# Optimization experiments

Hardware: AMD Instinct MI355X
Metric: run time of the kernel (lower is better)

The kernel has to match this reference:

```python
import jax, jax.numpy as jnp
import numpy as np

POOL = 7
IMAGE_SHAPE = (1024, 1024)
NUM_CLASSES = 81
BN_EPS = 1e-5


def _crop_and_resize(feat, boxes, P):
    """tf.image.crop_and_resize-style bilinear crop. feat: (B,C,H,W), boxes: (B,N,4) normalized [y1,x1,y2,x2]. Returns (B,N,C,P,P)."""
    B, C, H, W = feat.shape

    def one(f, bx):
        ff = f.reshape(C, H * W)
        y1, x1, y2, x2 = bx[:, 0], bx[:, 1], bx[:, 2], bx[:, 3]
        t = jnp.linspace(0.0, 1.0, P)
        ys = (y1[:, None] + (y2 - y1)[:, None] * t) * (H - 1)  # (N,P)
        xs = (x1[:, None] + (x2 - x1)[:, None] * t) * (W - 1)
        y0 = jnp.floor(ys)
        x0 = jnp.floor(xs)
        wy = (ys - y0)[None, :, :, None]  # broadcast to (1,N,P,1)
        wx = (xs - x0)[None, :, None, :]  # (1,N,1,P)
        yi0 = jnp.clip(y0, 0, H - 1).astype(jnp.int32)
        yi1 = jnp.clip(y0 + 1, 0, H - 1).astype(jnp.int32)
        xi0 = jnp.clip(x0, 0, W - 1).astype(jnp.int32)
        xi1 = jnp.clip(x0 + 1, 0, W - 1).astype(jnp.int32)

        def g(yi, xi):
            return ff[:, yi[:, :, None] * W + xi[:, None, :]]  # (C,N,P,P)

        out = (g(yi0, xi0) * (1 - wy) * (1 - wx) + g(yi0, xi1) * (1 - wy) * wx
               + g(yi1, xi0) * wy * (1 - wx) + g(yi1, xi1) * wy * wx)
        return jnp.transpose(out, (1, 0, 2, 3))  # (N,C,P,P)

    return jax.vmap(one)(feat, boxes)


def _pyramid_roi_align(rois, feats, P, image_shape):
    h = rois[..., 2] - rois[..., 0]
    w = rois[..., 3] - rois[..., 1]
    scale = 224.0 / np.sqrt(float(image_shape[0] * image_shape[1]))
    lvl = jnp.log2(jnp.sqrt(jnp.maximum(h * w, 1e-12)) / scale)
    level = jnp.clip(4 + jnp.round(lvl).astype(jnp.int32), 2, 5)  # (B,N)
    pooled = 0.0
    for i, f in enumerate(feats):  # levels 2..5
        mask = (level == (i + 2))[..., None, None, None].astype(f.dtype)
        pooled = pooled + mask * _crop_and_resize(f, rois, P)
    return pooled  # (B,N,C,P,P)


def _bn_relu(x, gamma, beta):
    # training-mode BatchNorm per batch slice (batch_slice => stats over the n_rois dim)
    mu = jnp.mean(x, axis=1, keepdims=True)
    var = jnp.mean((x - mu) ** 2, axis=1, keepdims=True)
    return jax.nn.relu(gamma * (x - mu) / jnp.sqrt(var + BN_EPS) + beta)


def setup_inputs() -> dict:
    key = jax.random.key(0)
    ks = jax.random.split(key, 16)
    B, N, C, F, K = 2, 1000, 256, 1024, NUM_CLASSES
    p = jax.random.uniform(ks[0], (B, N, 4), dtype=jnp.float32)
    yy = jnp.sort(p[..., 0:2], axis=-1)
    xx = jnp.sort(p[..., 2:4], axis=-1)
    rois = jnp.stack([yy[..., 0], xx[..., 0], yy[..., 1], xx[..., 1]], axis=-1)
    inp = {
        'rois': rois,
        'p2': jax.random.normal(ks[1], (B, C, 256, 256), dtype=jnp.float32),
        'p3': jax.random.normal(ks[2], (B, C, 128, 128), dtype=jnp.float32),
        'p4': jax.random.normal(ks[3], (B, C, 64, 64), dtype=jnp.float32),
        'p5': jax.random.normal(ks[4], (B, C, 32, 32), dtype=jnp.float32),
        'conv1_w': jax.random.normal(ks[5], (F, C, POOL, POOL), dtype=jnp.float32) * 0.02,
        'conv1_b': jnp.zeros((F,), jnp.float32),
        'bn1_g': jnp.ones((F,), jnp.float32),
        'bn1_b': jnp.zeros((F,), jnp.float32),
        'conv2_w': jax.random.normal(ks[6], (F, F), dtype=jnp.float32) * 0.02,
        'conv2_b': jnp.zeros((F,), jnp.float32),
        'bn2_g': jnp.ones((F,), jnp.float32),
        'bn2_b': jnp.zeros((F,), jnp.float32),
        'logits_w': jax.random.normal(ks[7], (K, F), dtype=jnp.float32) * 0.02,
        'logits_b': jnp.zeros((K,), jnp.float32),
        'bbox_w': jax.random.normal(ks[8], (K * 4, F), dtype=jnp.float32) * 0.02,
        'bbox_b': jnp.zeros((K * 4,), jnp.float32),
    }
    return inp


def reference(rois, p2, p3, p4, p5, conv1_w, conv1_b, bn1_g, bn1_b,
              conv2_w, conv2_b, bn2_g, bn2_b, logits_w, logits_b, bbox_w, bbox_b):
    B, N = rois.shape[0], rois.shape[1]
    pooled = _pyramid_roi_align(rois, [p2, p3, p4, p5], POOL, IMAGE_SHAPE)  # (B,N,C,P,P)
    # conv1: kernel == pool size => full contraction to 1x1 spatial
    x = jnp.einsum('bnchw,fchw->bnf', pooled, conv1_w) + conv1_b
    x = _bn_relu(x, bn1_g, bn1_b)
    # conv2: 1x1 conv == matmul
    x = x @ conv2_w.T + conv2_b
    shared = _bn_relu(x, bn2_g, bn2_b)  # (B,N,F)
    logits = shared @ logits_w.T + logits_b  # (B,N,K)
    probs = jax.nn.softmax(logits, axis=-1)
    bbox = (shared @ bbox_w.T + bbox_b).reshape(B, N, NUM_CLASSES, 4)
    return (logits, probs, bbox)
```

## Files before the change

kernel.cpp:

```cpp
#include <hip/hip_runtime.h>
#include <cstdint>
#include <cstddef>

typedef _Float16 H16;
typedef _Float16 half8 __attribute__((ext_vector_type(8)));
typedef float f32x4 __attribute__((ext_vector_type(4)));

typedef __attribute__((address_space(1))) const unsigned int gu32;
typedef __attribute__((address_space(3))) unsigned int lu32;
__device__ __forceinline__ void glds16(const void* g, void* l) {
  __builtin_amdgcn_global_load_lds((gu32*)g, (lu32*)l, 16, 0, 0);
}

__global__ __launch_bounds__(256) void k_transpose(const float* __restrict__ in,
                                                   H16* __restrict__ out,
                                                   int H, int W) {
  __shared__ float t[32 * 257];
  const int tid = threadIdx.x;
  const int w0 = blockIdx.x * 32;
  const int h  = blockIdx.y;
  const int b  = blockIdx.z;
  const size_t HW = (size_t)H * W;
  const int cL = tid >> 3;
  const int w4 = (tid & 7) * 4;
  const float* src = in + (size_t)b * 256 * HW + (size_t)h * W + w0;
#pragma unroll
  for (int i = 0; i < 8; ++i) {
    const int c = i * 32 + cL;
    const float4 v = *(const float4*)(src + (size_t)c * HW + w4);
    t[(w4 + 0) * 257 + c] = v.x;
    t[(w4 + 1) * 257 + c] = v.y;
    t[(w4 + 2) * 257 + c] = v.z;
    t[(w4 + 3) * 257 + c] = v.w;
  }
  __syncthreads();
  const int wS = (tid & 3) * 8;
  const int c4 = (tid >> 2) * 4;
  H16* dst = out + ((size_t)b * H + h) * W * 256;
#pragma unroll
  for (int j = 0; j < 8; ++j) {
    const int w = wS + j;
    const float a0 = t[w * 257 + c4 + 0];
    const float a1 = t[w * 257 + c4 + 1];
    const float a2 = t[w * 257 + c4 + 2];
    const float a3 = t[w * 257 + c4 + 3];
    union { H16 hh[4]; uint2 u; } r;
    r.hh[0] = (H16)a0; r.hh[1] = (H16)a1; r.hh[2] = (H16)a2; r.hh[3] = (H16)a3;
    *(uint2*)(dst + (size_t)(w0 + w) * 256 + c4) = r.u;
  }
}

__global__ __launch_bounds__(256) void k_prep_w1(const float* __restrict__ w,
                                                 H16* __restrict__ wt) {
  const int f = blockIdx.x;
  __shared__ __align__(16) H16 l[12544];
  const float* wf = w + (size_t)f * 12544;
  for (int e = threadIdx.x; e < 12544; e += 256) {
    const int cc = e / 49, pp = e % 49;
    l[pp * 256 + cc] = (H16)wf[e];
  }
  __syncthreads();
  H16* of = wt + (size_t)f * 12544;
  for (int ch = threadIdx.x; ch < 1568; ch += 256) {
    *(uint4*)(of + ch * 8) = *(const uint4*)(l + ch * 8);
  }
}

__global__ __launch_bounds__(256) void k_cast_f16(const float4* __restrict__ in,
                                                  uint2* __restrict__ out, int n4) {
  const int i = blockIdx.x * 256 + threadIdx.x;
  if (i >= n4) return;
  const float4 v = in[i];
  union { H16 hh[4]; uint2 u; } r;
  r.hh[0] = (H16)v.x; r.hh[1] = (H16)v.y; r.hh[2] = (H16)v.z; r.hh[3] = (H16)v.w;
  out[i] = r.u;
}

__global__ __launch_bounds__(256) void k_prep_w3(const float4* __restrict__ lw,
                                                 const float4* __restrict__ bw,
                                                 uint2* __restrict__ out) {
  const int i = blockIdx.x * 256 + threadIdx.x;
  const int r = (i * 4) >> 10;
  float4 v;
  if (r < 81)       v = lw[i];
  else if (r < 405) v = bw[i - 20736];
  else              v = make_float4(0.f, 0.f, 0.f, 0.f);
  union { H16 hh[4]; uint2 u; } rr;
  rr.hh[0] = (H16)v.x; rr.hh[1] = (H16)v.y; rr.hh[2] = (H16)v.z; rr.hh[3] = (H16)v.w;
  out[i] = rr.u;
}

__global__ __launch_bounds__(256) void k_roialign(const float* __restrict__ rois,
    const H16* __restrict__ f2, const H16* __restrict__ f3,
    const H16* __restrict__ f4p, const H16* __restrict__ f5,
    H16* __restrict__ pooled) {
  const int m = blockIdx.x;
  const int g  = threadIdx.x >> 6;
  const int c4 = (threadIdx.x & 63) * 4;
  H16* outp = pooled + (size_t)m * 12544 + c4;
  if (m >= 2000) {
    const uint2 z = make_uint2(0u, 0u);
    for (int p = g; p < 49; p += 4) *(uint2*)(outp + p * 256) = z;
    return;
  }
  const int b = (m >= 1000) ? 1 : 0;
  const float y1v = rois[m * 4 + 0], x1v = rois[m * 4 + 1];
  const float y2v = rois[m * 4 + 2], x2v = rois[m * 4 + 3];
  const float dy = y2v - y1v, dx = x2v - x1v;
  const float area = fmaxf(dy * dx, 1e-12f);
  const float lvl = log2f(sqrtf(area) / 0.21875f);
  int level = 4 + (int)rintf(lvl);
  level = level < 2 ? 2 : (level > 5 ? 5 : level);
  const H16* ft; int H;
  if (level == 2)      { ft = f2; H = 256; }
  else if (level == 3) { ft = f3; H = 128; }
  else if (level == 4) { ft = f4p; H = 64; }
  else                 { ft = f5; H = 32; }
  const float Hm1 = (float)(H - 1);
  const size_t bbase = (size_t)b * H * H * 256;
#pragma unroll 1
  for (int p = g; p < 49; p += 4) {
    const int py = (p * 147) >> 10;
    const int px = p - py * 7;
    const float ys = (y1v + dy * (py * 0.16666667f)) * Hm1;
    const float xs = (x1v + dx * (px * 0.16666667f)) * Hm1;
    const float yf = floorf(ys), xf = floorf(xs);
    const float wyv = ys - yf, wxv = xs - xf;
    int yi = (int)yf, xi = (int)xf;
    yi = yi < 0 ? 0 : (yi > H - 1 ? H - 1 : yi);
    xi = xi < 0 ? 0 : (xi > H - 1 ? H - 1 : xi);
    const int yiB = (yi + 1 > H - 1) ? H - 1 : yi + 1;
    const int xiB = (xi + 1 > H - 1) ? H - 1 : xi + 1;
    const size_t r0 = bbase + (size_t)yi * H * 256;
    const size_t r1 = bbase + (size_t)yiB * H * 256;
    union { uint2 u; H16 hh[4]; } v00, v01, v10, v11;
    v00.u = *(const uint2*)(ft + r0 + (size_t)xi  * 256 + c4);
    v01.u = *(const uint2*)(ft + r0 + (size_t)xiB * 256 + c4);
    v10.u = *(const uint2*)(ft + r1 + (size_t)xi  * 256 + c4);
    v11.u = *(const uint2*)(ft + r1 + (size_t)xiB * 256 + c4);
    const float w00 = (1.f - wyv) * (1.f - wxv);
    const float w01 = (1.f - wyv) * wxv;
    const float w10 = wyv * (1.f - wxv);
    const float w11 = wyv * wxv;
    union { H16 hh[4]; uint2 u; } r;
#pragma unroll
    for (int q = 0; q < 4; ++q) {
      const float val = (float)v00.hh[q] * w00 + (float)v01.hh[q] * w01
                      + (float)v10.hh[q] * w10 + (float)v11.hh[q] * w11;
      r.hh[q] = (H16)val;
    }
    *(uint2*)(outp + p * 256) = r.u;
  }
}

__global__ __launch_bounds__(256) void k_gemm(const H16* __restrict__ A,
                                              const H16* __restrict__ Bw,
                                              float* __restrict__ Cout,
                                              int Nn, int Ktot, int kchunk) {
  __shared__ __align__(16) H16 As[128 * 32];
  __shared__ __align__(16) H16 Bs[128 * 32];
  const int m0 = blockIdx.x * 128;
  const int n0 = blockIdx.y * 128;
  const int k0 = blockIdx.z * kchunk;
  float* __restrict__ Cp = Cout + (size_t)blockIdx.z * ((size_t)2048 * Nn);
  const int tid  = threadIdx.x;
  const int lane = tid & 63;
  const int wave = tid >> 6;
  const int wm = (wave >> 1) * 64;
  const int wn = (wave & 1) * 64;
  const int r1 = tid >> 2;
  const int cb = (tid & 3) * 8;
  const H16* gA1 = A  + (size_t)(m0 + r1) * Ktot + cb + k0;
  const H16* gA2 = A  + (size_t)(m0 + 64 + r1) * Ktot + cb + k0;
  const H16* gB1 = Bw + (size_t)(n0 + r1) * Ktot + cb + k0;
  const H16* gB2 = Bw + (size_t)(n0 + 64 + r1) * Ktot + cb + k0;
  H16* lA1 = As + tid * 8;
  H16* lA2 = As + 2048 + tid * 8;
  H16* lB1 = Bs + tid * 8;
  H16* lB2 = Bs + 2048 + tid * 8;
  f32x4 acc[4][4];
#pragma unroll
  for (int i = 0; i < 4; ++i)
#pragma unroll
    for (int j = 0; j < 4; ++j) acc[i][j] = (f32x4){0.f, 0.f, 0.f, 0.f};
  const int fr = lane & 15, fk = (lane >> 4) * 8;
  const int niter = kchunk >> 5;
  for (int it = 0; it < niter; ++it) {
    __syncthreads();
    glds16(gA1, lA1); glds16(gA2, lA2);
    glds16(gB1, lB1); glds16(gB2, lB2);
    gA1 += 32; gA2 += 32; gB1 += 32; gB2 += 32;
    __syncthreads();
    half8 af[4], bf[4];
#pragma unroll
    for (int i = 0; i < 4; ++i) af[i] = *(const half8*)(As + (wm + i * 16 + fr) * 32 + fk);
#pragma unroll
    for (int i = 0; i < 4; ++i) bf[i] = *(const half8*)(Bs + (wn + i * 16 + fr) * 32 + fk);
#pragma unroll
    for (int i = 0; i < 4; ++i)
#pragma unroll
      for (int j = 0; j < 4; ++j)
        acc[i][j] = __builtin_amdgcn_mfma_f32_16x16x32_f16(af[i], bf[j], acc[i][j], 0, 0, 0);
  }
  const int fq = lane >> 4;
#pragma unroll
  for (int i = 0; i < 4; ++i)
#pragma unroll
    for (int j = 0; j < 4; ++j) {
      const int col = n0 + wn + j * 16 + fr;
#pragma unroll
      for (int q = 0; q < 4; ++q) {
        const int row = m0 + wm + i * 16 + fq * 4 + q;
        Cp[(size_t)row * Nn + col] = acc[i][j][q];
      }
    }
}

__global__ __launch_bounds__(256) void k_reduce4(const float4* __restrict__ part,
                                                 float4* __restrict__ x1) {
  const int i = blockIdx.x * 256 + threadIdx.x;
  const float4 a = part[i], b = part[i + 524288], c = part[i + 1048576], d = part[i + 1572864];
  float4 r;
  r.x = a.x + b.x + c.x + d.x; r.y = a.y + b.y + c.y + d.y;
  r.z = a.z + b.z + c.z + d.z; r.w = a.w + b.w + c.w + d.w;
  x1[i] = r;
}

__global__ __launch_bounds__(256) void k_bn_stats(const float* __restrict__ X,
                                                  float* __restrict__ psum,
                                                  float* __restrict__ psq) {
  const int nc = blockIdx.x;
  const int b  = blockIdx.y;
  const int f4 = threadIdx.x * 4;
  const float* xp = X + (size_t)(b * 1000 + nc * 40) * 1024 + f4;
  float4 s = {0.f, 0.f, 0.f, 0.f}, q = {0.f, 0.f, 0.f, 0.f};
  for (int r = 0; r < 40; ++r) {
    const float4 v = *(const float4*)(xp + (size_t)r * 1024);
    s.x += v.x; s.y += v.y; s.z += v.z; s.w += v.w;
    q.x += v.x * v.x; q.y += v.y * v.y; q.z += v.z * v.z; q.w += v.w * v.w;
  }
  const size_t o = (size_t)(b * 25 + nc) * 1024 + f4;
  *(float4*)(psum + o) = s;
  *(float4*)(psq + o)  = q;
}

__global__ __launch_bounds__(256) void k_bn_fin(const float* __restrict__ psum,
                                                const float* __restrict__ psq,
                                                const float* __restrict__ gamma,
                                                const float* __restrict__ beta,
                                                float* __restrict__ coeff) {
  const int idx = blockIdx.x * 256 + threadIdx.x;
  const int b = idx >> 10, f = idx & 1023;
  float S = 0.f, Q = 0.f;
  for (int i = 0; i < 25; ++i) {
    S += psum[(size_t)(b * 25 + i) * 1024 + f];
    Q += psq[(size_t)(b * 25 + i) * 1024 + f];
  }
  const float mu   = S * 0.001f;
  const float var  = Q * 0.001f - mu * mu;
  const float rstd = rsqrtf(var + 1e-5f);
  const float a = gamma[f] * rstd;
  coeff[idx * 2]     = a;
  coeff[idx * 2 + 1] = beta[f] - mu * a;
}

__global__ __launch_bounds__(256) void k_bn_apply(const float* __restrict__ X,
                                                  const float* __restrict__ coeff,
                                                  H16* __restrict__ Y) {
  const int idx = blockIdx.x * 256 + threadIdx.x;
  const int m  = idx >> 8;
  const int f4 = (idx & 255) * 4;
  union { H16 hh[4]; uint2 u; } r;
  if (m >= 2000) {
    r.hh[0] = r.hh[1] = r.hh[2] = r.hh[3] = (H16)0.f;
    *(uint2*)(Y + (size_t)idx * 4) = r.u;
    return;
  }
  const int b = (m >= 1000) ? 1 : 0;
  const float4 v   = *(const float4*)(X + (size_t)idx * 4);
  const float4 c01 = *(const float4*)(coeff + b * 2048 + f4 * 2);
  const float4 c23 = *(const float4*)(coeff + b * 2048 + f4 * 2 + 4);
  r.hh[0] = (H16)fmaxf(c01.x * v.x + c01.y, 0.f);
  r.hh[1] = (H16)fmaxf(c01.z * v.y + c01.w, 0.f);
  r.hh[2] = (H16)fmaxf(c23.x * v.z + c23.y, 0.f);
  r.hh[3] = (H16)fmaxf(c23.z * v.w + c23.w, 0.f);
  *(uint2*)(Y + (size_t)idx * 4) = r.u;
}

__global__ __launch_bounds__(64) void k_head(const float* __restrict__ Z,
                                             const float* __restrict__ lb,
                                             const float* __restrict__ bb,
                                             float* __restrict__ out) {
  const int m = blockIdx.x;
  const int lane = threadIdx.x;
  const float* zr = Z + (size_t)m * 512;
  float* outL = out;
  float* outP = out + 162000;
  float* outB = out + 324000;
  const float v0 = zr[lane] + lb[lane];
  const float v1 = (lane < 17) ? (zr[64 + lane] + lb[64 + lane]) : -3.0e38f;
  outL[(size_t)m * 81 + lane] = v0;
  if (lane < 17) outL[(size_t)m * 81 + 64 + lane] = v1;
  float mx = fmaxf(v0, v1);
#pragma unroll
  for (int off = 32; off > 0; off >>= 1) mx = fmaxf(mx, __shfl_xor(mx, off));
  const float e0 = expf(v0 - mx);
  const float e1 = (lane < 17) ? expf(v1 - mx) : 0.f;
  float sm = e0 + e1;
#pragma unroll
  for (int off = 32; off > 0; off >>= 1) sm += __shfl_xor(sm, off);
  const float inv = 1.0f / sm;
  outP[(size_t)m * 81 + lane] = e0 * inv;
  if (lane < 17) outP[(size_t)m * 81 + 64 + lane] = e1 * inv;
#pragma unroll
  for (int j = 0; j < 6; ++j) {
    const int cc = lane + j * 64;
    if (cc < 324) outB[(size_t)m * 324 + cc] = zr[81 + cc] + bb[cc];
  }
}

extern "C" void kernel_launch(void* const* d_in, const int* in_sizes, int n_in,
                              void* d_out, int out_size, void* d_ws, size_t ws_size,
                              hipStream_t stream) {
  char* ws = (char*)d_ws;
  H16* fT2    = (H16*)(ws);
  H16* fT3    = (H16*)(ws + 67108864);
  H16* fT4    = (H16*)(ws + 83886080);
  H16* fT5    = (H16*)(ws + 88080384);
  H16* w1t    = (H16*)(ws + 89128960);
  H16* pooled = (H16*)(ws + 114819072);
  float* part  = (float*)(ws);
  float* x1    = (float*)(ws + 33554432);
  float* zz    = (float*)(ws + 41943040);
  H16*   y1    = (H16*)(ws + 67108864);
  float* x2    = (float*)(ws + 71303168);
  H16*   y2    = (H16*)(ws + 79691776);
  H16*   w2b   = (H16*)(ws + 83886080);
  H16*   w3b   = (H16*)(ws + 85983232);
  float* psum  = (float*)(ws + 87031808);
  float* psq   = (float*)(ws + 87236608);
  float* coef1 = (float*)(ws + 87441408);
  float* coef2 = (float*)(ws + 87457792);

  const float* rois = (const float*)d_in[0];

  k_transpose<<<dim3(8, 256, 2), 256, 0, stream>>>((const float*)d_in[1], fT2, 256, 256);
  k_transpose<<<dim3(4, 128, 2), 256, 0, stream>>>((const float*)d_in[2], fT3, 128, 128);
  k_transpose<<<dim3(2,  64, 2), 256, 0, stream>>>((const float*)d_in[3], fT4,  64,  64);
  k_transpose<<<dim3(1,  32, 2), 256, 0, stream>>>((const float*)d_in[4], fT5,  32,  32);
  k_prep_w1<<<1024, 256, 0, stream>>>((const float*)d_in[5], w1t);
  k_roialign<<<2048, 256, 0, stream>>>(rois, fT2, fT3, fT4, fT5, pooled);
  k_cast_f16<<<1024, 256, 0, stream>>>((const float4*)d_in[9], (uint2*)w2b, 262144);
  k_prep_w3<<<512, 256, 0, stream>>>((const float4*)d_in[13], (const float4*)d_in[15], (uint2*)w3b);

  k_gemm<<<dim3(16, 8, 4), 256, 0, stream>>>(pooled, w1t, part, 1024, 12544, 3136);
  k_reduce4<<<2048, 256, 0, stream>>>((const float4*)part, (float4*)x1);

  k_bn_stats<<<dim3(25, 2), 256, 0, stream>>>(x1, psum, psq);
  k_bn_fin<<<8, 256, 0, stream>>>(psum, psq, (const float*)d_in[7], (const float*)d_in[8], coef1);
  k_bn_apply<<<2048, 256, 0, stream>>>(x1, coef1, y1);

  k_gemm<<<dim3(16, 8, 1), 256, 0, stream>>>(y1, w2b, x2, 1024, 1024, 1024);

  k_bn_stats<<<dim3(25, 2), 256, 0, stream>>>(x2, psum, psq);
  k_bn_fin<<<8, 256, 0, stream>>>(psum, psq, (const float*)d_in[11], (const float*)d_in[12], coef2);
  k_bn_apply<<<2048, 256, 0, stream>>>(x2, coef2, y2);

  k_gemm<<<dim3(16, 4, 1), 256, 0, stream>>>(y2, w3b, zz, 512, 1024, 1024);
  k_head<<<2000, 64, 0, stream>>>(zz, (const float*)d_in[14], (const float*)d_in[16], (float*)d_out);
}
```

Before: 527.8 us.

## Increase split-K for all GEMMs, fuse reduction with BN stats, merge launches

The four per-level transposes become one launch, with a write pattern that stores each row contiguously, and the two small weight casts become one launch. The conv1 GEMM moves from 4 to 8 K-splits, and conv2 and the head GEMM get 4 K-splits each. The split-K partials are then summed inside a combined reduce+BN-stats kernel or inside the head kernel. The LDS padding in the w1 prep is changed to avoid bank conflicts. This is meant to fill more CUs during the small GEMMs and to cut launch count and extra passes over memory, at the cost of more partial-sum traffic.

```diff
diff --git a/kernel.cpp b/kernel.cpp
--- a/kernel.cpp
+++ b/kernel.cpp
@@ -12,18 +12,29 @@
   __builtin_amdgcn_global_load_lds((gu32*)g, (lu32*)l, 16, 0, 0);
 }
 
-__global__ __launch_bounds__(256) void k_transpose(const float* __restrict__ in,
-                                                   H16* __restrict__ out,
-                                                   int H, int W) {
+__global__ __launch_bounds__(256) void k_transpose_all(
+    const float* __restrict__ p2, const float* __restrict__ p3,
+    const float* __restrict__ p4, const float* __restrict__ p5,
+    H16* __restrict__ o2, H16* __restrict__ o3,
+    H16* __restrict__ o4, H16* __restrict__ o5) {
   __shared__ float t[32 * 257];
   const int tid = threadIdx.x;
-  const int w0 = blockIdx.x * 32;
-  const int h  = blockIdx.y;
-  const int b  = blockIdx.z;
-  const size_t HW = (size_t)H * W;
+  int bid = blockIdx.x;
+  const float* in; H16* out; int H;
+  if (bid < 4096)      { in = p2; out = o2; H = 256; }
+  else if (bid < 5120) { in = p3; out = o3; H = 128; bid -= 4096; }
+  else if (bid < 5376) { in = p4; out = o4; H = 64;  bid -= 5120; }
+  else                 { in = p5; out = o5; H = 32;  bid -= 5376; }
+  const int wpb = H >> 5;
+  const int strips = wpb * H;
+  const int b = (bid >= strips) ? 1 : 0;
+  bid -= b ? strips : 0;
+  const int h = bid / wpb;
+  const int w0 = (bid - h * wpb) * 32;
+  const size_t HW = (size_t)H * H;
   const int cL = tid >> 3;
   const int w4 = (tid & 7) * 4;
-  const float* src = in + (size_t)b * 256 * HW + (size_t)h * W + w0;
+  const float* src = in + (size_t)b * 256 * HW + (size_t)h * H + w0;
 #pragma unroll
   for (int i = 0; i < 8; ++i) {
     const int c = i * 32 + cL;
@@ -34,60 +45,60 @@
     t[(w4 + 3) * 257 + c] = v.w;
   }
   __syncthreads();
-  const int wS = (tid & 3) * 8;
-  const int c4 = (tid >> 2) * 4;
-  H16* dst = out + ((size_t)b * H + h) * W * 256;
+  const int wS = tid >> 6;
+  const int c4 = (tid & 63) * 4;
+  H16* dst = out + (((size_t)b * H + h) * H + w0) * 256;
 #pragma unroll
   for (int j = 0; j < 8; ++j) {
-    const int w = wS + j;
-    const float a0 = t[w * 257 + c4 + 0];
-    const float a1 = t[w * 257 + c4 + 1];
-    const float a2 = t[w * 257 + c4 + 2];
-    const float a3 = t[w * 257 + c4 + 3];
+    const int w = wS + j * 4;
     union { H16 hh[4]; uint2 u; } r;
-    r.hh[0] = (H16)a0; r.hh[1] = (H16)a1; r.hh[2] = (H16)a2; r.hh[3] = (H16)a3;
-    *(uint2*)(dst + (size_t)(w0 + w) * 256 + c4) = r.u;
+    r.hh[0] = (H16)t[w * 257 + c4 + 0];
+    r.hh[1] = (H16)t[w * 257 + c4 + 1];
+    r.hh[2] = (H16)t[w * 257 + c4 + 2];
+    r.hh[3] = (H16)t[w * 257 + c4 + 3];
+    *(uint2*)(dst + (size_t)w * 256 + c4) = r.u;
   }
 }
 
 __global__ __launch_bounds__(256) void k_prep_w1(const float* __restrict__ w,
                                                  H16* __restrict__ wt) {
   const int f = blockIdx.x;
-  __shared__ __align__(16) H16 l[12544];
+  __shared__ __align__(16) H16 l[49 * 264];
   const float* wf = w + (size_t)f * 12544;
   for (int e = threadIdx.x; e < 12544; e += 256) {
-    const int cc = e / 49, pp = e % 49;
-    l[pp * 256 + cc] = (H16)wf[e];
+    const int cc = e / 49, pp = e - cc * 49;
+    l[pp * 264 + cc] = (H16)wf[e];
   }
   __syncthreads();
   H16* of = wt + (size_t)f * 12544;
   for (int ch = threadIdx.x; ch < 1568; ch += 256) {
-    *(uint4*)(of + ch * 8) = *(const uint4*)(l + ch * 8);
-  }
-}
-
-__global__ __launch_bounds__(256) void k_cast_f16(const float4* __restrict__ in,
-                                                  uint2* __restrict__ out, int n4) {
-  const int i = blockIdx.x * 256 + threadIdx.x;
-  if (i >= n4) return;
-  const float4 v = in[i];
+    const int p = ch >> 5, c8 = (ch & 31) * 8;
+    *(uint4*)(of + (ch << 3)) = *(const uint4*)(l + p * 264 + c8);
+  }
+}
+
+__global__ __launch_bounds__(256) void k_prep_small(const float4* __restrict__ w2,
+                                                    const float4* __restrict__ lw,
+                                                    const float4* __restrict__ bw,
+                                                    uint2* __restrict__ w2b,
+                                                    uint2* __restrict__ w3b) {
+  const int bid = blockIdx.x;
   union { H16 hh[4]; uint2 u; } r;
-  r.hh[0] = (H16)v.x; r.hh[1] = (H16)v.y; r.hh[2] = (H16)v.z; r.hh[3] = (H16)v.w;
-  out[i] = r.u;
-}
-
-__global__ __launch_bounds__(256) void k_prep_w3(const float4* __restrict__ lw,
-                                                 const float4* __restrict__ bw,
-                                                 uint2* __restrict__ out) {
-  const int i = blockIdx.x * 256 + threadIdx.x;
-  const int r = (i * 4) >> 10;
-  float4 v;
-  if (r < 81)       v = lw[i];
-  else if (r < 405) v = bw[i - 20736];
-  else              v = make_float4(0.f, 0.f, 0.f, 0.f);
-  union { H16 hh[4]; uint2 u; } rr;
-  rr.hh[0] = (H16)v.x; rr.hh[1] = (H16)v.y; rr.hh[2] = (H16)v.z; rr.hh[3] = (H16)v.w;
-  out[i] = rr.u;
+  if (bid < 1024) {
+    const int i = bid * 256 + threadIdx.x;
+    const float4 v = w2[i];
+    r.hh[0] = (H16)v.x; r.hh[1] = (H16)v.y; r.hh[2] = (H16)v.z; r.hh[3] = (H16)v.w;
+    w2b[i] = r.u;
+  } else {
+    const int i = (bid - 1024) * 256 + threadIdx.x;
+    const int row = (i * 4) >> 10;
+    float4 v;
+    if (row < 81)       v = lw[i];
+    else if (row < 405) v = bw[i - 20736];
+    else                v = make_float4(0.f, 0.f, 0.f, 0.f);
+    r.hh[0] = (H16)v.x; r.hh[1] = (H16)v.y; r.hh[2] = (H16)v.z; r.hh[3] = (H16)v.w;
+    w3b[i] = r.u;
+  }
 }
 
 __global__ __launch_bounds__(256) void k_roialign(const float* __restrict__ rois,
@@ -216,32 +227,28 @@
     }
 }
 
-__global__ __launch_bounds__(256) void k_reduce4(const float4* __restrict__ part,
-                                                 float4* __restrict__ x1) {
-  const int i = blockIdx.x * 256 + threadIdx.x;
-  const float4 a = part[i], b = part[i + 524288], c = part[i + 1048576], d = part[i + 1572864];
-  float4 r;
-  r.x = a.x + b.x + c.x + d.x; r.y = a.y + b.y + c.y + d.y;
-  r.z = a.z + b.z + c.z + d.z; r.w = a.w + b.w + c.w + d.w;
-  x1[i] = r;
-}
-
-__global__ __launch_bounds__(256) void k_bn_stats(const float* __restrict__ X,
-                                                  float* __restrict__ psum,
-                                                  float* __restrict__ psq) {
-  const int nc = blockIdx.x;
-  const int b  = blockIdx.y;
+__global__ __launch_bounds__(256) void k_red_stats(const float* __restrict__ part,
+                                                   float* __restrict__ X,
+                                                   float* __restrict__ psum,
+                                                   float* __restrict__ psq,
+                                                   int nz) {
+  const int chunk = blockIdx.x;
+  const int r0 = chunk * 8;
   const int f4 = threadIdx.x * 4;
-  const float* xp = X + (size_t)(b * 1000 + nc * 40) * 1024 + f4;
-  float4 s = {0.f, 0.f, 0.f, 0.f}, q = {0.f, 0.f, 0.f, 0.f};
-  for (int r = 0; r < 40; ++r) {
-    const float4 v = *(const float4*)(xp + (size_t)r * 1024);
-    s.x += v.x; s.y += v.y; s.z += v.z; s.w += v.w;
-    q.x += v.x * v.x; q.y += v.y * v.y; q.z += v.z * v.z; q.w += v.w * v.w;
-  }
-  const size_t o = (size_t)(b * 25 + nc) * 1024 + f4;
-  *(float4*)(psum + o) = s;
-  *(float4*)(psq + o)  = q;
+  f32x4 s = {0.f, 0.f, 0.f, 0.f}, q = {0.f, 0.f, 0.f, 0.f};
+#pragma unroll 1
+  for (int r = 0; r < 8; ++r) {
+    const size_t row = r0 + r;
+    f32x4 a = {0.f, 0.f, 0.f, 0.f};
+    for (int z = 0; z < nz; ++z) {
+      const f32x4 v = *(const f32x4*)(part + ((size_t)z * 2048 + row) * 1024 + f4);
+      a += v;
+    }
+    *(f32x4*)(X + row * 1024 + f4) = a;
+    s += a; q += a * a;
+  }
+  *(f32x4*)(psum + (size_t)chunk * 1024 + f4) = s;
+  *(f32x4*)(psq  + (size_t)chunk * 1024 + f4) = q;
 }
 
 __global__ __launch_bounds__(256) void k_bn_fin(const float* __restrict__ psum,
@@ -252,9 +259,9 @@
   const int idx = blockIdx.x * 256 + threadIdx.x;
   const int b = idx >> 10, f = idx & 1023;
   float S = 0.f, Q = 0.f;
-  for (int i = 0; i < 25; ++i) {
-    S += psum[(size_t)(b * 25 + i) * 1024 + f];
-    Q += psq[(size_t)(b * 25 + i) * 1024 + f];
+  for (int i = 0; i < 125; ++i) {
+    S += psum[(size_t)(b * 125 + i) * 1024 + f];
+    Q += psq[(size_t)(b * 125 + i) * 1024 + f];
   }
   const float mu   = S * 0.001f;
   const float var  = Q * 0.001f - mu * mu;
@@ -287,18 +294,23 @@
   *(uint2*)(Y + (size_t)idx * 4) = r.u;
 }
 
-__global__ __launch_bounds__(64) void k_head(const float* __restrict__ Z,
+__global__ __launch_bounds__(64) void k_head(const float* __restrict__ Zp,
                                              const float* __restrict__ lb,
                                              const float* __restrict__ bb,
                                              float* __restrict__ out) {
   const int m = blockIdx.x;
   const int lane = threadIdx.x;
-  const float* zr = Z + (size_t)m * 512;
+  const size_t P = (size_t)2048 * 512;
+  const float* zr = Zp + (size_t)m * 512;
   float* outL = out;
   float* outP = out + 162000;
   float* outB = out + 324000;
-  const float v0 = zr[lane] + lb[lane];
-  const float v1 = (lane < 17) ? (zr[64 + lane] + lb[64 + lane]) : -3.0e38f;
+  const float v0 = zr[lane] + zr[P + lane] + zr[2 * P + lane] + zr[3 * P + lane] + lb[lane];
+  float v1 = -3.0e38f;
+  if (lane < 17) {
+    const int c = 64 + lane;
+    v1 = zr[c] + zr[P + c] + zr[2 * P + c] + zr[3 * P + c] + lb[c];
+  }
   outL[(size_t)m * 81 + lane] = v0;
   if (lane < 17) outL[(size_t)m * 81 + 64 + lane] = v1;
   float mx = fmaxf(v0, v1);
@@ -315,7 +327,10 @@
 #pragma unroll
   for (int j = 0; j < 6; ++j) {
     const int cc = lane + j * 64;
-    if (cc < 324) outB[(size_t)m * 324 + cc] = zr[81 + cc] + bb[cc];
+    if (cc < 324) {
+      const int c = 81 + cc;
+      outB[(size_t)m * 324 + cc] = zr[c] + zr[P + c] + zr[2 * P + c] + zr[3 * P + c] + bb[cc];
+    }
   }
 }
 
@@ -329,43 +344,40 @@
   H16* fT5    = (H16*)(ws + 88080384);
   H16* w1t    = (H16*)(ws + 89128960);
   H16* pooled = (H16*)(ws + 114819072);
-  float* part  = (float*)(ws);
-  float* x1    = (float*)(ws + 33554432);
-  float* zz    = (float*)(ws + 41943040);
-  H16*   y1    = (H16*)(ws + 67108864);
-  float* x2    = (float*)(ws + 71303168);
-  H16*   y2    = (H16*)(ws + 79691776);
+  float* part1 = (float*)(ws);
+  float* x1    = (float*)(ws + 67108864);
+  H16*   y1    = (H16*)(ws + 75497472);
   H16*   w2b   = (H16*)(ws + 83886080);
   H16*   w3b   = (H16*)(ws + 85983232);
   float* psum  = (float*)(ws + 87031808);
-  float* psq   = (float*)(ws + 87236608);
-  float* coef1 = (float*)(ws + 87441408);
-  float* coef2 = (float*)(ws + 87457792);
+  float* psq   = (float*)(ws + 88055808);
+  float* coef1 = (float*)(ws + 89079808);
+  float* coef2 = (float*)(ws + 89096192);
+  float* x2    = (float*)(ws + 89128960);
+  H16*   y2    = (H16*)(ws + 97517568);
+  float* part2 = (float*)(ws + 114819072);
+  float* zhead = (float*)(ws);
 
   const float* rois = (const float*)d_in[0];
 
-  k_transpose<<<dim3(8, 256, 2), 256, 0, stream>>>((const float*)d_in[1], fT2, 256, 256);
-  k_transpose<<<dim3(4, 128, 2), 256, 0, stream>>>((const float*)d_in[2], fT3, 128, 128);
-  k_transpose<<<dim3(2,  64, 2), 256, 0, stream>>>((const float*)d_in[3], fT4,  64,  64);
-  k_transpose<<<dim3(1,  32, 2), 256, 0, stream>>>((const float*)d_in[4], fT5,  32,  32);
+  k_transpose_all<<<5440, 256, 0, stream>>>(
+      (const float*)d_in[1], (const float*)d_in[2],
+      (const float*)d_in[3], (const float*)d_in[4], fT2, fT3, fT4, fT5);
   k_prep_w1<<<1024, 256, 0, stream>>>((const float*)d_in[5], w1t);
   k_roialign<<<2048, 256, 0, stream>>>(rois, fT2, fT3, fT4, fT5, pooled);
-  k_cast_f16<<<1024, 256, 0, stream>>>((const float4*)d_in[9], (uint2*)w2b, 262144);
-  k_prep_w3<<<512, 256, 0, stream>>>((const float4*)d_in[13], (const float4*)d_in[15], (uint2*)w3b);
-
-  k_gemm<<<dim3(16, 8, 4), 256, 0, stream>>>(pooled, w1t, part, 1024, 12544, 3136);
-  k_reduce4<<<2048, 256, 0, stream>>>((const float4*)part, (float4*)x1);
-
-  k_bn_stats<<<dim3(25, 2), 256, 0, stream>>>(x1, psum, psq);
+  k_prep_small<<<1536, 256, 0, stream>>>((const float4*)d_in[9],
+      (const float4*)d_in[13], (const float4*)d_in[15], (uint2*)w2b, (uint2*)w3b);
+
+  k_gemm<<<dim3(16, 8, 8), 256, 0, stream>>>(pooled, w1t, part1, 1024, 12544, 1568);
+  k_red_stats<<<250, 256, 0, stream>>>(part1, x1, psum, psq, 8);
   k_bn_fin<<<8, 256, 0, stream>>>(psum, psq, (const float*)d_in[7], (const float*)d_in[8], coef1);
   k_bn_apply<<<2048, 256, 0, stream>>>(x1, coef1, y1);
 
-  k_gemm<<<dim3(16, 8, 1), 256, 0, stream>>>(y1, w2b, x2, 1024, 1024, 1024);
-
-  k_bn_stats<<<dim3(25, 2), 256, 0, stream>>>(x2, psum, psq);
+  k_gemm<<<dim3(16, 8, 4), 256, 0, stream>>>(y1, w2b, part2, 1024, 1024, 256);
+  k_red_stats<<<250, 256, 0, stream>>>(part2, x2, psum, psq, 4);
   k_bn_fin<<<8, 256, 0, stream>>>(psum, psq, (const float*)d_in[11], (const float*)d_in[12], coef2);
   k_bn_apply<<<2048, 256, 0, stream>>>(x2, coef2, y2);
 
-  k_gemm<<<dim3(16, 4, 1), 256, 0, stream>>>(y2, w3b, zz, 512, 1024, 1024);
-  k_head<<<2000, 64, 0, stream>>>(zz, (const float*)d_in[14], (const float*)d_in[16], (float*)d_out);
-}
+  k_gemm<<<dim3(16, 4, 4), 256, 0, stream>>>(y2, w3b, zhead, 512, 1024, 256);
+  k_head<<<2000, 64, 0, stream>>>(zhead, (const float*)d_in[14], (const float*)d_in[16], (float*)d_out);
+}
```

Result: faster. 505.2 us (-4.3%).
